# Kernel optimization log

Measured on AMD Instinct MI355X. Metric: run time of the kernel, lower is better.

The kernel has to match this reference:

```python
import jax, jax.numpy as jnp
import numpy as np

B, L, C, H, W = 8, 8, 64, 56, 56
K = 3
EPS = 1e-5


def setup_inputs() -> dict:
    key = jax.random.key(0)
    ks = jax.random.split(key, 7)
    s = lambda k, shape, sc=0.05: jax.random.normal(k, shape, dtype=jnp.float32) * sc
    return {
        "x": jax.random.normal(ks[0], (B, L, C, H, W), dtype=jnp.float32),
        "temporal_w": s(ks[1], (C, C)),        # Conv3d 1x1x1 C->C
        "temporal_b": s(ks[2], (C,)),
        "fc_w": s(ks[3], (C,)),                # Conv3d 1x1x1 C->1
        "fc_b": s(ks[4], (1,)),
        "conv_w": s(ks[5], (C, C, K, K), 0.1), # self.weight [1,1,Co,Ci,k,k] core
        "conv_b": s(ks[6], (C,)),              # self.bias [1,1,Co] core
        "bn_gamma": jnp.ones((C,), jnp.float32),
        "bn_beta": jnp.zeros((C,), jnp.float32),
    }


def reference(x, temporal_w, temporal_b, fc_w, fc_b, conv_w, conv_b, bn_gamma, bn_beta):
    b, l, c, h, w = x.shape
    # ---- generateweight_fourier ----
    xin = jnp.transpose(x, (0, 2, 1, 3, 4))                # [B,C,L,H,W]
    f = jnp.fft.fft2(xin, axes=(3, 4), norm='ortho')       # spatial FFT
    f = jnp.fft.fft(f, axis=2, norm='ortho')               # temporal FFT
    allxin = xin + 0.01 * jnp.abs(f) * xin                 # Fourier2 attention + residual
    pooled = allxin.mean(axis=(3, 4))                      # AdaptiveAvgPool3d((None,1,1)) -> [B,C,L]
    # temporalconv: 1x1x1 Conv3d C->C on [B,C,L,1,1]
    calib = jnp.einsum('oc,bcl->bol', temporal_w, pooled) + temporal_b[None, :, None]  # [B,C,L]
    # fc: 1x1x1 Conv3d C->1
    fcout = jnp.einsum('c,bcl->bl', fc_w, pooled) + fc_b[0]                            # [B,L]
    # finalweight: weight[1,1,Co,Ci,k,k] * (calib+1) broadcast over Ci -> [B,L,Co,Ci,k,k]
    calib_blc = jnp.transpose(calib, (0, 2, 1)) + 1.0      # [B,L,Ci]
    fw = conv_w[None, None] * calib_blc[:, :, None, :, None, None]
    fb = conv_b[None, None, :] * (fcout + 1.0)[:, :, None] # [B,L,Co]
    # ---- dynamic per-(sample,frame) conv2d (groups = b*l) ----
    x_flat = x.reshape(b * l, c, h, w)
    fw_flat = fw.reshape(b * l, c, c, K, K)
    fb_flat = fb.reshape(b * l, c)

    def per_sample(xi, wi):
        return jax.lax.conv_general_dilated(
            xi[None], wi, window_strides=(1, 1), padding=[(1, 1), (1, 1)],
            dimension_numbers=('NCHW', 'OIHW', 'NCHW'))[0]

    out = jax.vmap(per_sample)(x_flat, fw_flat) + fb_flat[:, :, None, None]
    out = x_flat + out                                     # residual (gate=False)
    # BatchNorm2d (training-mode batch statistics)
    mean = out.mean(axis=(0, 2, 3), keepdims=True)
    var = out.var(axis=(0, 2, 3), keepdims=True)
    out = (out - mean) * jax.lax.rsqrt(var + EPS)
    out = out * bn_gamma[None, :, None, None] + bn_beta[None, :, None, None]
    out = out * jax.nn.sigmoid(out)                        # SiLU
    return out.reshape(b, l, c, h, w)
```

## Files before the change

### kernel.cpp

```cpp
#include <hip/hip_runtime.h>
#include <cmath>

#define HW 3136
#define NF 64
#define NBLK2 448

typedef __attribute__((ext_vector_type(8))) short short8;
typedef __attribute__((ext_vector_type(4))) float float4a;

__device__ __forceinline__ unsigned short f2bf(float f) {
    unsigned int u = __float_as_uint(f);
    u += 0x7fffu + ((u >> 16) & 1u);
    return (unsigned short)(u >> 16);
}
__device__ __forceinline__ float bf2f(unsigned short u) {
    return __uint_as_float(((unsigned int)u) << 16);
}

__global__ __launch_bounds__(256)
void pack_kernel(const float* __restrict__ cw,
                 unsigned short* __restrict__ Ffix,
                 unsigned short* __restrict__ Wp) {
    if (blockIdx.x < 64) {
        int idx = blockIdx.x * 256 + threadIdx.x;
        int j    = idx & 7;
        int lane = (idx >> 3) & 63;
        int ks   = (idx >> 9) & 3;
        int t    = (idx >> 11) & 3;
        int p    = (idx >> 13) & 1;
        int mn = t * 16 + (lane & 15);
        int k  = ks * 32 + (lane >> 4) * 8 + j;
        float val = 0.f;
        if (mn < 56 && k < 112) {
            int kk = (k < 56) ? k : k - 56;
            int prod = (mn * kk) % 56;
            float ang = -6.2831853071795864f * (float)prod / 56.0f;
            float cr = cosf(ang);
            float ci = sinf(ang);
            float first  = (p == 0) ? cr : ci;
            float second = (p == 0) ? -ci : cr;
            val = (k < 56) ? first : second;
        }
        Ffix[idx] = f2bf(val);
    } else {
        int idx = (blockIdx.x - 64) * 256 + threadIdx.x;
        if (idx < 36864) {
            int i  = idx & 63;
            int o  = (idx >> 6) & 63;
            int kk = idx >> 12;
            Wp[idx] = f2bf(cw[(o * 64 + i) * 9 + kk]);
        }
    }
}

__global__ __launch_bounds__(512, 4)
void fft_mfma_kernel(const float* __restrict__ x,
                     const unsigned short* __restrict__ Ffix,
                     float* __restrict__ pooled) {
    const int bc = blockIdx.x;
    const int c  = bc & 63;
    const int b  = bc >> 6;
    const int tid  = threadIdx.x;
    const int lane = tid & 63;
    const int wv   = tid >> 6;
    const int n    = lane & 15;
    const int q    = lane >> 4;

    __shared__ unsigned short sh[40320];
    unsigned short* xbf = sh;
    unsigned short* Tb  = sh + 25088;
    unsigned short* Ub  = sh + 25088 + 56 * 136;
    float* G = (float*)(sh + 25088);
    __shared__ float xsum[8];
    __shared__ float red[16];

    for (int t = tid; t < 6272; t += 512) {
        int l = t / 784, r = t - l * 784;
        float4 v = *(const float4*)(x + ((size_t)((b * 8 + l) * 64 + c)) * HW + r * 4);
        ushort4 o;
        o.x = f2bf(v.x); o.y = f2bf(v.y); o.z = f2bf(v.z); o.w = f2bf(v.w);
        *(ushort4*)(xbf + l * 3136 + r * 4) = o;
    }
    __syncthreads();

    {
        float s = 0.f;
        for (int i = lane; i < 3136; i += 64) s += bf2f(xbf[wv * 3136 + i]);
        #pragma unroll
        for (int m = 1; m < 64; m <<= 1) s += __shfl_xor(s, m);
        if (lane == 0) xsum[wv] = s;
    }

    #pragma unroll 1
    for (int lp = 0; lp < 5; ++lp) {
        for (int t = tid; t < 1344; t += 512) {
            int row = t / 12;
            ((unsigned int*)(sh + 25088))[row * 68 + 56 + (t - row * 12)] = 0u;
        }

        float tr[8], ti[8];
        #pragma unroll
        for (int l = 0; l < 8; ++l) {
            float ang = -0.78539816339744831f * (float)((l * lp) & 7);
            tr[l] = cosf(ang);
            ti[l] = sinf(ang);
        }
        for (int s = tid; s < 784; s += 512) {
            int h = s / 14, w4 = s - h * 14;
            float re[4] = {0.f, 0.f, 0.f, 0.f}, im[4] = {0.f, 0.f, 0.f, 0.f};
            #pragma unroll
            for (int l = 0; l < 8; ++l) {
                ushort4 u = *(const ushort4*)(xbf + l * 3136 + h * 56 + w4 * 4);
                float v0 = bf2f(u.x), v1 = bf2f(u.y), v2 = bf2f(u.z), v3 = bf2f(u.w);
                re[0] += v0 * tr[l]; im[0] += v0 * ti[l];
                re[1] += v1 * tr[l]; im[1] += v1 * ti[l];
                re[2] += v2 * tr[l]; im[2] += v2 * ti[l];
                re[3] += v3 * tr[l]; im[3] += v3 * ti[l];
            }
            #pragma unroll
            for (int j = 0; j < 4; ++j) {
                int w = w4 * 4 + j;
                Tb[w * 136 + h]      = f2bf(re[j]);
                Tb[w * 136 + 56 + h] = f2bf(im[j]);
            }
        }
        __syncthreads();

        {
            const int p  = wv >> 2;
            const int mt = wv & 3;
            float4a s1[4];
            #pragma unroll
            for (int nt = 0; nt < 4; ++nt) s1[nt] = (float4a){0.f, 0.f, 0.f, 0.f};
            #pragma unroll
            for (int ks = 0; ks < 4; ++ks) {
                short8 afr = *(const short8*)(Ffix + ((((p * 4 + mt) * 4 + ks) * 64 + lane) * 8));
                #pragma unroll
                for (int nt = 0; nt < 4; ++nt) {
                    int row = nt * 16 + n; if (row > 55) row = 55;
                    short8 bfr = *(const short8*)(Tb + row * 136 + ks * 32 + q * 8);
                    s1[nt] = __builtin_amdgcn_mfma_f32_16x16x32_bf16(afr, bfr, s1[nt], 0, 0, 0);
                }
            }
            #pragma unroll
            for (int nt = 0; nt < 4; ++nt)
                #pragma unroll
                for (int r = 0; r < 4; ++r) {
                    int kh = mt * 16 + q * 4 + r;
                    int w  = nt * 16 + n;
                    if (kh < 56 && w < 56)
                        Ub[kh * 136 + p * 56 + w] = f2bf(s1[nt][r]);
                }
        }
        __syncthreads();

        const int mt = wv & 3;
        const int pp = wv >> 2;
        short8 afr2[4];
        #pragma unroll
        for (int ks = 0; ks < 4; ++ks) {
            int row = mt * 16 + n; if (row > 55) row = 55;
            afr2[ks] = *(const short8*)(Ub + row * 136 + ks * 32 + q * 8);
        }
        float4a g[4];
        #pragma unroll
        for (int nt = 0; nt < 4; ++nt) g[nt] = (float4a){0.f, 0.f, 0.f, 0.f};
        #pragma unroll
        for (int ks = 0; ks < 4; ++ks)
            #pragma unroll
            for (int nt = 0; nt < 4; ++nt) {
                short8 bfr = *(const short8*)(Ffix + ((((pp * 4 + nt) * 4 + ks) * 64 + lane) * 8));
                g[nt] = __builtin_amdgcn_mfma_f32_16x16x32_bf16(afr2[ks], bfr, g[nt], 0, 0, 0);
            }
        __syncthreads();

        #pragma unroll
        for (int nt = 0; nt < 4; ++nt) {
            int kw = nt * 16 + n;
            #pragma unroll
            for (int r = 0; r < 4; ++r) {
                int kh = mt * 16 + q * 4 + r;
                if (kh < 56 && kw < 56)
                    G[pp * 3192 + kh * 57 + kw] = g[nt][r];
            }
        }
        __syncthreads();

        const bool doflip = (lp >= 1 && lp <= 3);
        const unsigned short* x1 = xbf + lp * 3136;
        const unsigned short* x2 = xbf + ((8 - lp) & 7) * 3136;
        float S1 = 0.f, S2 = 0.f;
        for (int t = tid; t < 3136; t += 512) {
            int kh = t / 56;
            int kw = t - kh * 56;
            float gr = G[kh * 57 + kw];
            float gi = G[3192 + kh * 57 + kw];
            float mag = sqrtf(gr * gr + gi * gi);
            S1 += mag * bf2f(x1[t]);
            if (doflip) {
                int khf = kh ? 56 - kh : 0;
                int kwf = kw ? 56 - kw : 0;
                S2 += mag * bf2f(x2[khf * 56 + kwf]);
            }
        }
        #pragma unroll
        for (int m = 1; m < 64; m <<= 1) {
            S1 += __shfl_xor(S1, m);
            S2 += __shfl_xor(S2, m);
        }
        if (lane == 0) { red[wv * 2] = S1; red[wv * 2 + 1] = S2; }
        __syncthreads();
        if (tid == 0) {
            float s1 = 0.f, s2 = 0.f;
            #pragma unroll
            for (int w = 0; w < 8; ++w) { s1 += red[w * 2]; s2 += red[w * 2 + 1]; }
            const float kS = 0.01f / (56.0f * 2.8284271247461903f);
            pooled[bc * 8 + lp] = (xsum[lp] + kS * s1) / 3136.0f;
            if (doflip)
                pooled[bc * 8 + (8 - lp)] = (xsum[8 - lp] + kS * s2) / 3136.0f;
        }
        __syncthreads();
    }
}

__global__ __launch_bounds__(64)
void calib_kernel(const float* __restrict__ pooled,
                  const float* __restrict__ tw_, const float* __restrict__ tb,
                  const float* __restrict__ fcw, const float* __restrict__ fcb,
                  const float* __restrict__ convb,
                  float* __restrict__ scale, float* __restrict__ fbias) {
    const int nn = blockIdx.x;
    const int b = nn >> 3, l = nn & 7;
    const int o = threadIdx.x;
    const float* pr = pooled + b * 512 + l;
    float dot = 0.f;
    #pragma unroll 8
    for (int c0 = 0; c0 < 64; ++c0) dot += tw_[o * 64 + c0] * pr[c0 * 8];
    float fcp = fcw[o] * pr[o * 8];
    #pragma unroll
    for (int off = 32; off > 0; off >>= 1) fcp += __shfl_down(fcp, off);
    float fcout = __shfl(fcp, 0) + fcb[0];
    scale[nn * 64 + o] = 1.0f + tb[o] + dot;
    fbias[nn * 64 + o] = convb[o] * (fcout + 1.0f);
}

__global__ __launch_bounds__(256, 2)
void conv_mfma_kernel(const float* __restrict__ x,
                      const unsigned short* __restrict__ Wp,
                      const float* __restrict__ scale, const float* __restrict__ fbias,
                      float* __restrict__ out,
                      float* __restrict__ psum, float* __restrict__ psum2) {
    const int rt = blockIdx.x;
    const int nn = blockIdx.y;
    const int tid  = threadIdx.x;
    const int lane = tid & 63;
    const int wv   = tid >> 6;
    const int r0   = rt * 8;

    __shared__ unsigned short xs[10 * 60 * 64];
    __shared__ float fb[64], ssc[64], rsc[64], bn1[64], bn2[64];

    if (tid < 64) {
        fb[tid]  = fbias[nn * 64 + tid];
        float s  = scale[nn * 64 + tid];
        ssc[tid] = s;
        rsc[tid] = 1.0f / s;
        bn1[tid] = 0.f; bn2[tid] = 0.f;
    }
    __syncthreads();

    for (int t = tid; t < 10240; t += 256) {
        if (t < 8960) {
            int c4 = t % 14;
            int rr = (t / 14) % 10;
            int i  = t / 140;
            int gr = r0 - 1 + rr;
            float4 v = make_float4(0.f, 0.f, 0.f, 0.f);
            if (gr >= 0 && gr < 56)
                v = *(const float4*)(x + ((size_t)(nn * 64 + i) * HW + gr * 56 + c4 * 4));
            float s = ssc[i];
            int g = i >> 3, il = i & 7;
            float vv[4] = {v.x, v.y, v.z, v.w};
            #pragma unroll
            for (int j = 0; j < 4; ++j) {
                int lc = c4 * 4 + 1 + j;
                xs[(rr * 60 + lc) * 64 + (((g ^ (lc & 7)) << 3) | il)] = f2bf(vv[j] * s);
            }
        } else {
            int idx = t - 8960;
            int i   = idx / 20;
            int rem = idx - i * 20;
            int rr  = rem >> 1;
            int lc  = (rem & 1) * 57;
            int g = i >> 3, il = i & 7;
            xs[(rr * 60 + lc) * 64 + (((g ^ (lc & 7)) << 3) | il)] = 0;
        }
    }
    __syncthreads();

    const int pxo = lane & 15;
    const int q   = lane >> 4;

    float4a acc[7][4];
    #pragma unroll
    for (int j = 0; j < 7; ++j)
        #pragma unroll
        for (int ot = 0; ot < 4; ++ot) acc[j][ot] = (float4a){0.f, 0.f, 0.f, 0.f};

    int rp[7], cp[7];
    #pragma unroll
    for (int j = 0; j < 7; ++j) {
        int px = (wv * 7 + j) * 16 + pxo;
        rp[j] = px / 56;
        cp[j] = px - rp[j] * 56;
    }

    #pragma unroll 1
    for (int kk = 0; kk < 9; ++kk) {
        const int dr = kk / 3, dc = kk - dr * 3;
        short8 a[4][2];
        #pragma unroll
        for (int ot = 0; ot < 4; ++ot)
            #pragma unroll
            for (int ih = 0; ih < 2; ++ih)
                a[ot][ih] = *(const short8*)(Wp + ((kk * 64 + ot * 16 + pxo) * 64 + ih * 32 + q * 8));

        #pragma unroll
        for (int j = 0; j < 7; ++j) {
            int lc = cp[j] + dc;
            int base = ((rp[j] + dr) * 60 + lc) * 64;
            int sw = lc & 7;
            #pragma unroll
            for (int ih = 0; ih < 2; ++ih) {
                short8 bv = *(const short8*)&xs[base + (((q + ih * 4) ^ sw) << 3)];
                #pragma unroll
                for (int ot = 0; ot < 4; ++ot)
                    acc[j][ot] = __builtin_amdgcn_mfma_f32_16x16x32_bf16(a[ot][ih], bv, acc[j][ot], 0, 0, 0);
            }
        }
    }

    float bs[4][4], bs2[4][4];
    #pragma unroll
    for (int ot = 0; ot < 4; ++ot)
        #pragma unroll
        for (int r = 0; r < 4; ++r) { bs[ot][r] = 0.f; bs2[ot][r] = 0.f; }

    #pragma unroll
    for (int j = 0; j < 7; ++j) {
        int px  = (wv * 7 + j) * 16 + pxo;
        int gpx = r0 * 56 + px;
        int rr  = rp[j] + 1;
        int lc  = cp[j] + 1;
        int sw  = lc & 7;
        int rowbase = (rr * 60 + lc) * 64;
        #pragma unroll
        for (int ot = 0; ot < 4; ++ot) {
            int g  = ot * 2 + (q >> 1);
            ushort4 uu = *(const ushort4*)(xs + rowbase + (((g ^ sw) << 3) | ((q & 1) * 4)));
            float resid[4] = {bf2f(uu.x), bf2f(uu.y), bf2f(uu.z), bf2f(uu.w)};
            #pragma unroll
            for (int r = 0; r < 4; ++r) {
                int o = ot * 16 + q * 4 + r;
                size_t off = (size_t)(nn * 64 + o) * HW + gpx;
                float v = acc[j][ot][r] + resid[r] * rsc[o] + fb[o];
                out[off] = v;
                bs[ot][r]  += v;
                bs2[ot][r] += v * v;
            }
        }
    }
    #pragma unroll
    for (int ot = 0; ot < 4; ++ot)
        #pragma unroll
        for (int r = 0; r < 4; ++r) {
            #pragma unroll
            for (int m = 1; m < 16; m <<= 1) {
                bs[ot][r]  += __shfl_xor(bs[ot][r], m);
                bs2[ot][r] += __shfl_xor(bs2[ot][r], m);
            }
        }
    if (pxo == 0) {
        #pragma unroll
        for (int ot = 0; ot < 4; ++ot)
            #pragma unroll
            for (int r = 0; r < 4; ++r) {
                int o = ot * 16 + q * 4 + r;
                atomicAdd(&bn1[o], bs[ot][r]);
                atomicAdd(&bn2[o], bs2[ot][r]);
            }
    }
    __syncthreads();
    if (tid < 64) {
        int bl = nn * 7 + rt;
        psum[bl * 64 + tid]  = bn1[tid];
        psum2[bl * 64 + tid] = bn2[tid];
    }
}

__global__ __launch_bounds__(256)
void bnstat_kernel(const float* __restrict__ psum, const float* __restrict__ psum2,
                   float* __restrict__ bn) {
    const int o = blockIdx.x;
    const int tid = threadIdx.x;
    float s = 0.f, s2 = 0.f;
    for (int bl = tid; bl < NBLK2; bl += 256) {
        s  += psum[bl * 64 + o];
        s2 += psum2[bl * 64 + o];
    }
    __shared__ float r1[256], r2[256];
    r1[tid] = s; r2[tid] = s2;
    __syncthreads();
    for (int st = 128; st > 0; st >>= 1) {
        if (tid < st) { r1[tid] += r1[tid + st]; r2[tid] += r2[tid + st]; }
        __syncthreads();
    }
    if (tid == 0) {
        const float N = 64.0f * (float)HW;
        float mean = r1[0] / N;
        float var  = r2[0] / N - mean * mean;
        bn[o]      = mean;
        bn[64 + o] = rsqrtf(var + 1e-5f);
    }
}

__global__ __launch_bounds__(256)
void bnsilu_kernel(float* __restrict__ out, const float* __restrict__ bn,
                   const float* __restrict__ gamma, const float* __restrict__ beta) {
    size_t idx = (size_t)blockIdx.x * 256 + threadIdx.x;
    if (idx >= (size_t)NF * 64 * HW) return;
    int c = (int)((idx / HW) & 63);
    float v = out[idx];
    float y = (v - bn[c]) * bn[64 + c] * gamma[c] + beta[c];
    out[idx] = y / (1.0f + expf(-y));
}

extern "C" void kernel_launch(void* const* d_in, const int* in_sizes, int n_in,
                              void* d_out, int out_size, void* d_ws, size_t ws_size,
                              hipStream_t stream) {
    const float* x          = (const float*)d_in[0];
    const float* temporal_w = (const float*)d_in[1];
    const float* temporal_b = (const float*)d_in[2];
    const float* fc_w       = (const float*)d_in[3];
    const float* fc_b       = (const float*)d_in[4];
    const float* conv_w     = (const float*)d_in[5];
    const float* conv_b     = (const float*)d_in[6];
    const float* bn_gamma   = (const float*)d_in[7];
    const float* bn_beta    = (const float*)d_in[8];
    float* out = (float*)d_out;
    float* ws  = (float*)d_ws;

    float* pooled = ws;
    float* scale  = ws + 4096;
    float* fbias  = ws + 8192;
    unsigned short* Wp = (unsigned short*)(ws + 12288);
    float* psum   = ws + 12288 + 18432;
    float* psum2  = psum + NBLK2 * 64;
    float* bn     = psum2 + NBLK2 * 64;
    unsigned short* Ffix = (unsigned short*)(bn + 128);

    pack_kernel<<<208, 256, 0, stream>>>(conv_w, Ffix, Wp);
    fft_mfma_kernel<<<512, 512, 0, stream>>>(x, Ffix, pooled);
    calib_kernel<<<64, 64, 0, stream>>>(pooled, temporal_w, temporal_b,
                                        fc_w, fc_b, conv_b, scale, fbias);
    conv_mfma_kernel<<<dim3(7, 64), 256, 0, stream>>>(x, Wp, scale, fbias,
                                                      out, psum, psum2);
    bnstat_kernel<<<64, 256, 0, stream>>>(psum, psum2, bn);
    int total = NF * 64 * HW;
    bnsilu_kernel<<<(total + 255) / 256, 256, 0, stream>>>(out, bn, bn_gamma, bn_beta);
}
```

Measured before the change: 236.9 us.

## Consume second-stage FFT MFMA results in registers instead of staging through LDS

The second MFMA stage is reorganised so each wave computes both real and imaginary parts for its own tile. The magnitude-times-x reduction then reads directly from the accumulator registers, which removes the G shared-memory round trip and two barriers per loop iteration. Zero-padding of the shared scratch now happens once before the loop, a trailing barrier is dropped, and the 4-blocks-per-CU occupancy hint is removed. In exchange, the Ffix loads per wave double and register pressure may rise, which could lower occupancy.

Result: slower. 244.2 us (+3.1%).

```diff
diff --git a/kernel.cpp b/kernel.cpp
--- a/kernel.cpp
+++ b/kernel.cpp
@@ -53,7 +53,7 @@
     }
 }
 
-__global__ __launch_bounds__(512, 4)
+__global__ __launch_bounds__(512)
 void fft_mfma_kernel(const float* __restrict__ x,
                      const unsigned short* __restrict__ Ffix,
                      float* __restrict__ pooled) {
@@ -70,9 +70,11 @@
     unsigned short* xbf = sh;
     unsigned short* Tb  = sh + 25088;
     unsigned short* Ub  = sh + 25088 + 56 * 136;
-    float* G = (float*)(sh + 25088);
     __shared__ float xsum[8];
     __shared__ float red[16];
+
+    for (int t = tid; t < 7616; t += 512)
+        ((unsigned int*)(sh + 25088))[t] = 0u;
 
     for (int t = tid; t < 6272; t += 512) {
         int l = t / 784, r = t - l * 784;
@@ -93,11 +95,6 @@
 
     #pragma unroll 1
     for (int lp = 0; lp < 5; ++lp) {
-        for (int t = tid; t < 1344; t += 512) {
-            int row = t / 12;
-            ((unsigned int*)(sh + 25088))[row * 68 + 56 + (t - row * 12)] = 0u;
-        }
-
         float tr[8], ti[8];
         #pragma unroll
         for (int l = 0; l < 8; ++l) {
@@ -155,52 +152,51 @@
         __syncthreads();
 
         const int mt = wv & 3;
-        const int pp = wv >> 2;
+        const int nh = wv >> 2;
         short8 afr2[4];
         #pragma unroll
         for (int ks = 0; ks < 4; ++ks) {
             int row = mt * 16 + n; if (row > 55) row = 55;
             afr2[ks] = *(const short8*)(Ub + row * 136 + ks * 32 + q * 8);
         }
-        float4a g[4];
-        #pragma unroll
-        for (int nt = 0; nt < 4; ++nt) g[nt] = (float4a){0.f, 0.f, 0.f, 0.f};
-        #pragma unroll
-        for (int ks = 0; ks < 4; ++ks)
-            #pragma unroll
-            for (int nt = 0; nt < 4; ++nt) {
-                short8 bfr = *(const short8*)(Ffix + ((((pp * 4 + nt) * 4 + ks) * 64 + lane) * 8));
-                g[nt] = __builtin_amdgcn_mfma_f32_16x16x32_bf16(afr2[ks], bfr, g[nt], 0, 0, 0);
-            }
-        __syncthreads();
-
-        #pragma unroll
-        for (int nt = 0; nt < 4; ++nt) {
-            int kw = nt * 16 + n;
-            #pragma unroll
-            for (int r = 0; r < 4; ++r) {
-                int kh = mt * 16 + q * 4 + r;
-                if (kh < 56 && kw < 56)
-                    G[pp * 3192 + kh * 57 + kw] = g[nt][r];
-            }
-        }
-        __syncthreads();
+        float4a g[2][2];
+        #pragma unroll
+        for (int pp = 0; pp < 2; ++pp)
+            #pragma unroll
+            for (int u = 0; u < 2; ++u) g[pp][u] = (float4a){0.f, 0.f, 0.f, 0.f};
+        #pragma unroll
+        for (int pp = 0; pp < 2; ++pp)
+            #pragma unroll
+            for (int ks = 0; ks < 4; ++ks)
+                #pragma unroll
+                for (int u = 0; u < 2; ++u) {
+                    int nt = nh * 2 + u;
+                    short8 bfr = *(const short8*)(Ffix + ((((pp * 4 + nt) * 4 + ks) * 64 + lane) * 8));
+                    g[pp][u] = __builtin_amdgcn_mfma_f32_16x16x32_bf16(afr2[ks], bfr, g[pp][u], 0, 0, 0);
+                }
 
         const bool doflip = (lp >= 1 && lp <= 3);
         const unsigned short* x1 = xbf + lp * 3136;
         const unsigned short* x2 = xbf + ((8 - lp) & 7) * 3136;
         float S1 = 0.f, S2 = 0.f;
-        for (int t = tid; t < 3136; t += 512) {
-            int kh = t / 56;
-            int kw = t - kh * 56;
-            float gr = G[kh * 57 + kw];
-            float gi = G[3192 + kh * 57 + kw];
-            float mag = sqrtf(gr * gr + gi * gi);
-            S1 += mag * bf2f(x1[t]);
-            if (doflip) {
-                int khf = kh ? 56 - kh : 0;
+        #pragma unroll
+        for (int u = 0; u < 2; ++u) {
+            int kw = (nh * 2 + u) * 16 + n;
+            if (kw < 56) {
                 int kwf = kw ? 56 - kw : 0;
-                S2 += mag * bf2f(x2[khf * 56 + kwf]);
+                #pragma unroll
+                for (int r = 0; r < 4; ++r) {
+                    int kh = mt * 16 + q * 4 + r;
+                    if (kh < 56) {
+                        float gr = g[0][u][r], gi = g[1][u][r];
+                        float mag = sqrtf(gr * gr + gi * gi);
+                        S1 += mag * bf2f(x1[kh * 56 + kw]);
+                        if (doflip) {
+                            int khf = kh ? 56 - kh : 0;
+                            S2 += mag * bf2f(x2[khf * 56 + kwf]);
+                        }
+                    }
+                }
             }
         }
         #pragma unroll
@@ -219,7 +215,6 @@
             if (doflip)
                 pooled[bc * 8 + (8 - lp)] = (xsum[8 - lp] + kS * s2) / 3136.0f;
         }
-        __syncthreads();
     }
 }
 
```
